# Optimization experiments

Hardware: AMD Instinct MI355X
Metric: run time of the kernel (lower is better)

## Reference

```python
import jax, jax.numpy as jnp
import numpy as np

SLOPE = 0.2  # LeakyReLU negative slope

def _mlp2(x, w1, b1, w2, b2):
    h = jax.nn.leaky_relu(x @ w1 + b1, SLOPE)
    return h @ w2 + b2

def setup_inputs() -> dict:
    key = jax.random.key(0)
    ks = jax.random.split(key, 16)
    B, N, T, A, H = 8, 512, 8, 16, 64
    D = T * A  # node_dim * timestep = 128
    s = 0.1
    return {
        "nodes": jax.random.normal(ks[0], (B, N, T, A), dtype=jnp.float32),
        "edges": jax.random.randint(ks[1], (B, N, N), 0, 2),
        "self_w1": jax.random.normal(ks[2], (D, H), dtype=jnp.float32) * s,
        "self_b1": jnp.zeros((H,), jnp.float32),
        "self_w2": jax.random.normal(ks[3], (H, H), dtype=jnp.float32) * s,
        "self_b2": jnp.zeros((H,), jnp.float32),
        "nb_w1": jax.random.normal(ks[4], (D, H), dtype=jnp.float32) * s,
        "nb_b1": jnp.zeros((H,), jnp.float32),
        "nb_w2": jax.random.normal(ks[5], (H, H), dtype=jnp.float32) * s,
        "nb_b2": jnp.zeros((H,), jnp.float32),
        "comb_w1": jax.random.normal(ks[6], (2 * H, H), dtype=jnp.float32) * s,
        "comb_b1": jnp.zeros((H,), jnp.float32),
        "comb_w2": jax.random.normal(ks[7], (H, 1), dtype=jnp.float32) * s,
        "comb_b2": jnp.zeros((1,), jnp.float32),
    }

def reference(nodes, edges, self_w1, self_b1, self_w2, self_b2,
              nb_w1, nb_b1, nb_w2, nb_b2,
              comb_w1, comb_b1, comb_w2, comb_b2):
    B, N = nodes.shape[0], nodes.shape[1]
    H = self_w2.shape[1]
    x = nodes.reshape(B, N, -1)                       # [B,N,D]
    self_e = _mlp2(x, self_w1, self_b1, self_w2, self_b2)  # [B,N,H]
    nb_e = _mlp2(x, nb_w1, nb_b1, nb_w2, nb_b2)            # [B,N,H]

    # combine_mlp(cat(self_i, nb_j)) scores; split fc1 to avoid [B,N,N,2H]
    w1_s, w1_n = comb_w1[:H], comb_w1[H:]
    pre = (jnp.einsum('bih,hk->bik', self_e, w1_s)[:, :, None, :]
           + jnp.einsum('bjh,hk->bjk', nb_e, w1_n)[:, None, :, :]
           + comb_b1)                                  # [B,N,N,H] (i=target, j=neighbor)
    scores = (jax.nn.leaky_relu(pre, SLOPE) @ comb_w2)[..., 0] + comb_b2[0]  # [B,N,N]

    # mask[b,i,j] = edges[b,j,i] != 0 and i != j
    mask = (jnp.swapaxes(edges, 1, 2) != 0) & (~jnp.eye(N, dtype=bool))
    neg = jnp.finfo(scores.dtype).min
    weights = jax.nn.softmax(jnp.where(mask, scores, neg), axis=-1)
    weights = jnp.where(mask, weights, 0.0)

    agg = jnp.einsum('bij,bjh->bih', weights, nb_e)    # weighted neighbor sum
    has_nb = mask.any(-1)                              # nodes w/o neighbors stay zero
    return jnp.where(has_nb[..., None], agg + self_e, 0.0)
```

## Files before the change

kernel.cpp:

```cpp
#include <hip/hip_runtime.h>
#include <float.h>

typedef __attribute__((ext_vector_type(8))) short short8;
typedef __attribute__((ext_vector_type(4))) float f32x4;

#define SLOPE 0.2f

__device__ __forceinline__ float leaky(float x) { return fmaxf(x, SLOPE * x); }

__device__ __forceinline__ unsigned short f2bf(float f) {
  unsigned u = __float_as_uint(f);
  return (unsigned short)((u + 0x7FFFu + ((u >> 16) & 1u)) >> 16);
}

__global__ __launch_bounds__(64) void wprep(
    const float* __restrict__ self_w1, const float* __restrict__ self_w2,
    const float* __restrict__ nb_w1,   const float* __restrict__ nb_w2,
    const float* __restrict__ comb_w1,
    unsigned short* __restrict__ wf)
{
  const int frag = blockIdx.x;
  const int lane = threadIdx.x;
  const int p = frag >> 5, fl = frag & 31;
  const float* src;
  int nt, kb;
  if (fl < 16)      { src = p ? nb_w1 : self_w1; nt = fl >> 2;        kb = fl & 3; }
  else if (fl < 24) { src = p ? nb_w2 : self_w2; nt = (fl - 16) >> 1; kb = (fl - 16) & 1; }
  else              { src = comb_w1 + p * 4096;  nt = (fl - 24) >> 1; kb = (fl - 24) & 1; }
  const int n = nt * 16 + (lane & 15);
  const int k0 = kb * 32 + (lane >> 4) * 8;
  short8 pk;
  #pragma unroll
  for (int j = 0; j < 8; ++j) pk[j] = (short)f2bf(src[(k0 + j) * 64 + n]);
  *(short8*)(wf + ((size_t)(frag * 64 + lane)) * 8) = pk;
}

__global__ __launch_bounds__(64) void mlp(
    const float* __restrict__ nodes,
    const float* __restrict__ self_b1, const float* __restrict__ self_b2,
    const float* __restrict__ nb_b1,   const float* __restrict__ nb_b2,
    const float* __restrict__ comb_b1, const float* __restrict__ comb_w2,
    const float* __restrict__ comb_b2,
    const unsigned short* __restrict__ wf,
    float* __restrict__ self_e, float* __restrict__ ss, float* __restrict__ sn,
    float* __restrict__ sP, float* __restrict__ sQ,
    unsigned short* __restrict__ nbT)
{
  __shared__ float tile[16][68];

  const int lane = threadIdx.x;
  const int arow = lane & 15, agrp = lane >> 4;
  const int node0 = blockIdx.x * 16;
  const int b = node0 >> 9, jloc = node0 & 511;

  short8 xa[4];
  {
    const float* xrow = nodes + ((size_t)(node0 + arow)) * 128 + agrp * 8;
    #pragma unroll
    for (int kb = 0; kb < 4; ++kb) {
      float v[8];
      *(float4*)&v[0] = *(const float4*)(xrow + kb * 32);
      *(float4*)&v[4] = *(const float4*)(xrow + kb * 32 + 4);
      #pragma unroll
      for (int j = 0; j < 8; ++j) xa[kb][j] = (short)f2bf(v[j]);
    }
  }

  float w2vn[4], cb1v[4];
  #pragma unroll
  for (int nt = 0; nt < 4; ++nt) {
    w2vn[nt] = comb_w2[nt * 16 + arow];
    cb1v[nt] = comb_b1[nt * 16 + arow];
  }
  const float cb2 = comb_b2[0];

  for (int p = 0; p < 2; ++p) {
    const float* b1 = p ? nb_b1 : self_b1;
    const float* b2 = p ? nb_b2 : self_b2;
    const unsigned short* wfp = wf + (size_t)p * 32 * 64 * 8;

    short8 w1f[16], w2f[8], cwf[8];
    #pragma unroll
    for (int i = 0; i < 16; ++i)
      w1f[i] = *(const short8*)(wfp + ((size_t)(i * 64 + lane)) * 8);
    #pragma unroll
    for (int i = 0; i < 8; ++i)
      w2f[i] = *(const short8*)(wfp + ((size_t)((16 + i) * 64 + lane)) * 8);
    #pragma unroll
    for (int i = 0; i < 8; ++i)
      cwf[i] = *(const short8*)(wfp + ((size_t)((24 + i) * 64 + lane)) * 8);

    f32x4 acc[4];
    #pragma unroll
    for (int nt = 0; nt < 4; ++nt) acc[nt] = (f32x4){0.f, 0.f, 0.f, 0.f};
    #pragma unroll
    for (int kb = 0; kb < 4; ++kb)
      #pragma unroll
      for (int nt = 0; nt < 4; ++nt)
        acc[nt] = __builtin_amdgcn_mfma_f32_16x16x32_bf16(xa[kb], w1f[nt * 4 + kb], acc[nt], 0, 0, 0);
    #pragma unroll
    for (int nt = 0; nt < 4; ++nt) {
      const float bv = b1[nt * 16 + arow];
      #pragma unroll
      for (int r = 0; r < 4; ++r)
        tile[agrp * 4 + r][nt * 16 + arow] = leaky(acc[nt][r] + bv);
    }

    short8 ha[2];
    #pragma unroll
    for (int kb = 0; kb < 2; ++kb) {
      float v[8];
      *(float4*)&v[0] = *(const float4*)&tile[arow][kb * 32 + agrp * 8];
      *(float4*)&v[4] = *(const float4*)&tile[arow][kb * 32 + agrp * 8 + 4];
      #pragma unroll
      for (int j = 0; j < 8; ++j) ha[kb][j] = (short)f2bf(v[j]);
    }

    #pragma unroll
    for (int nt = 0; nt < 4; ++nt) acc[nt] = (f32x4){0.f, 0.f, 0.f, 0.f};
    #pragma unroll
    for (int kb = 0; kb < 2; ++kb)
      #pragma unroll
      for (int nt = 0; nt < 4; ++nt)
        acc[nt] = __builtin_amdgcn_mfma_f32_16x16x32_bf16(ha[kb], w2f[nt * 2 + kb], acc[nt], 0, 0, 0);
    #pragma unroll
    for (int nt = 0; nt < 4; ++nt) {
      const float bv = b2[nt * 16 + arow];
      #pragma unroll
      for (int r = 0; r < 4; ++r) {
        const float ev = acc[nt][r] + bv;
        tile[agrp * 4 + r][nt * 16 + arow] = ev;
        if (p == 0)
          self_e[((size_t)(node0 + agrp * 4 + r)) * 64 + nt * 16 + arow] = ev;
      }
    }

    short8 ea[2];
    #pragma unroll
    for (int kb = 0; kb < 2; ++kb) {
      float v[8];
      *(float4*)&v[0] = *(const float4*)&tile[arow][kb * 32 + agrp * 8];
      *(float4*)&v[4] = *(const float4*)&tile[arow][kb * 32 + agrp * 8 + 4];
      #pragma unroll
      for (int j = 0; j < 8; ++j) ea[kb][j] = (short)f2bf(v[j]);
    }

    if (p == 1) {
      #pragma unroll
      for (int g = 0; g < 2; ++g) {
        short8 pk;
        #pragma unroll
        for (int jj = 0; jj < 8; ++jj)
          pk[jj] = (short)f2bf(tile[g * 8 + jj][lane]);
        *(short8*)(nbT + (size_t)b * 32768 + ((size_t)((jloc >> 3) + g)) * 512 + lane * 8) = pk;
      }
    }

    #pragma unroll
    for (int nt = 0; nt < 4; ++nt) acc[nt] = (f32x4){0.f, 0.f, 0.f, 0.f};
    #pragma unroll
    for (int kb = 0; kb < 2; ++kb)
      #pragma unroll
      for (int nt = 0; nt < 4; ++nt)
        acc[nt] = __builtin_amdgcn_mfma_f32_16x16x32_bf16(ea[kb], cwf[nt * 2 + kb], acc[nt], 0, 0, 0);

    float* so = p ? sn : ss;
    float t[4] = {0.f, 0.f, 0.f, 0.f};
    #pragma unroll
    for (int nt = 0; nt < 4; ++nt) {
      #pragma unroll
      for (int r = 0; r < 4; ++r) {
        const float sv = acc[nt][r] + (p ? 0.f : cb1v[nt]);
        so[((size_t)(node0 + agrp * 4 + r)) * 64 + nt * 16 + arow] = sv;
        t[r] += w2vn[nt] * sv;
      }
    }
    #pragma unroll
    for (int r = 0; r < 4; ++r) {
      #pragma unroll
      for (int off = 1; off < 16; off <<= 1) t[r] += __shfl_xor(t[r], off);
    }
    if (arow == 0) {
      float* po = p ? sQ : sP;
      const float add = p ? 0.f : cb2;
      #pragma unroll
      for (int r = 0; r < 4; ++r)
        po[node0 + agrp * 4 + r] = 0.6f * t[r] + add;
    }
  }
}

__global__ __launch_bounds__(512) void gat_attn(
    const int* __restrict__ edges,
    const float* __restrict__ comb_w2,
    const float* __restrict__ self_e,
    const float* __restrict__ ss, const float* __restrict__ sn,
    const float* __restrict__ sP, const float* __restrict__ sQ,
    const unsigned short* __restrict__ nbT,
    float* __restrict__ out)
{
  __shared__ __align__(16) float sn_sh[2][64][68];
  __shared__ __align__(16) unsigned short P_sh[16][520];
  __shared__ __align__(16) float red_sh[4][64][4];
  __shared__ unsigned short jm_sh[512];
  __shared__ float f_sh[16];

  const int tid = threadIdx.x, lane = tid & 63, wv = tid >> 6;
  const int b = blockIdx.x & 7, it = blockIdx.x >> 3;
  const int i0 = it * 16;
  const size_t nodeb = (size_t)b * 512;

  const int ra = wv * 2, rb = ra + 1;
  const int ia = i0 + ra, ib = ia + 1;

  const int* ebp = edges + ((size_t)(nodeb + tid)) * 512 + i0;
  const int4 ev0 = *(const int4*)(ebp + 0);
  const int4 ev1 = *(const int4*)(ebp + 4);
  const int4 ev2 = *(const int4*)(ebp + 8);
  const int4 ev3 = *(const int4*)(ebp + 12);

  float4 w2p[16], sa0[16], sa1[16];
  {
    const float4* w2v = (const float4*)comb_w2;
    const float4* s0 = (const float4*)(ss + (nodeb + ia) * 64);
    const float4* s1 = (const float4*)(ss + (nodeb + ib) * 64);
    #pragma unroll
    for (int q = 0; q < 16; ++q) {
      float4 w = w2v[q];
      w2p[q] = make_float4(0.4f * w.x, 0.4f * w.y, 0.4f * w.z, 0.4f * w.w);
      sa0[q] = s0[q];
      sa1[q] = s1[q];
    }
  }
  const float sPa = sP[nodeb + ia], sPb = sP[nodeb + ib];
  float sQv[8];
  #pragma unroll
  for (int jt = 0; jt < 8; ++jt) sQv[jt] = sQ[nodeb + jt * 64 + lane];

  {
    unsigned mj = 0;
    mj |= (ev0.x != 0 ? 1u : 0u) << 0;  mj |= (ev0.y != 0 ? 1u : 0u) << 1;
    mj |= (ev0.z != 0 ? 1u : 0u) << 2;  mj |= (ev0.w != 0 ? 1u : 0u) << 3;
    mj |= (ev1.x != 0 ? 1u : 0u) << 4;  mj |= (ev1.y != 0 ? 1u : 0u) << 5;
    mj |= (ev1.z != 0 ? 1u : 0u) << 6;  mj |= (ev1.w != 0 ? 1u : 0u) << 7;
    mj |= (ev2.x != 0 ? 1u : 0u) << 8;  mj |= (ev2.y != 0 ? 1u : 0u) << 9;
    mj |= (ev2.z != 0 ? 1u : 0u) << 10; mj |= (ev2.w != 0 ? 1u : 0u) << 11;
    mj |= (ev3.x != 0 ? 1u : 0u) << 12; mj |= (ev3.y != 0 ? 1u : 0u) << 13;
    mj |= (ev3.z != 0 ? 1u : 0u) << 14; mj |= (ev3.w != 0 ? 1u : 0u) << 15;
    const int d = tid - i0;
    if (d >= 0 && d < 16) mj &= ~(1u << d);
    jm_sh[tid] = (unsigned short)mj;
  }

  const int str = tid >> 4, stc = (tid & 15) * 4;
  const int str2 = (tid + 512) >> 4, stc2 = ((tid + 512) & 15) * 4;
  float4 st0, st1;
  {
    const float4* src = (const float4*)(sn + nodeb * 64);
    st0 = src[tid];
    st1 = src[tid + 512];
  }

  float msc0[8], msc1[8];
  int cur = 0;
  for (int jt = 0; jt < 8; ++jt) {
    *(float4*)&sn_sh[cur][str][stc] = st0;
    *(float4*)&sn_sh[cur][str2][stc2] = st1;
    if (jt < 7) {
      const float4* src = (const float4*)(sn + (nodeb + (jt + 1) * 64) * 64);
      st0 = src[tid];
      st1 = src[tid + 512];
    }
    __syncthreads();

    float acc0 = 0.f, acc1 = 0.f;
    #pragma unroll
    for (int q = 0; q < 16; ++q) {
      float4 v = *(const float4*)&sn_sh[cur][lane][q * 4];
      float4 w = w2p[q];
      float4 A = sa0[q];
      float4 Bv = sa1[q];
      acc0 += w.x * fabsf(A.x + v.x) + w.y * fabsf(A.y + v.y)
            + w.z * fabsf(A.z + v.z) + w.w * fabsf(A.w + v.w);
      acc1 += w.x * fabsf(Bv.x + v.x) + w.y * fabsf(Bv.y + v.y)
            + w.z * fabsf(Bv.z + v.z) + w.w * fabsf(Bv.w + v.w);
    }
    const unsigned mj = jm_sh[jt * 64 + lane];
    msc0[jt] = ((mj >> ra) & 1u) ? acc0 + sPa + sQv[jt] : -FLT_MAX;
    msc1[jt] = ((mj >> rb) & 1u) ? acc1 + sPb + sQv[jt] : -FLT_MAX;
    cur ^= 1;
  }

  float m0 = msc0[0], m1 = msc1[0];
  #pragma unroll
  for (int jt = 1; jt < 8; ++jt) {
    m0 = fmaxf(m0, msc0[jt]);
    m1 = fmaxf(m1, msc1[jt]);
  }
  #pragma unroll
  for (int off = 32; off; off >>= 1) {
    m0 = fmaxf(m0, __shfl_xor(m0, off));
    m1 = fmaxf(m1, __shfl_xor(m1, off));
  }

  float s0 = 0.f, s1 = 0.f;
  #pragma unroll
  for (int jt = 0; jt < 8; ++jt) {
    const float e0 = __expf(msc0[jt] - m0);
    const float e1 = __expf(msc1[jt] - m1);
    P_sh[ra][jt * 64 + lane] = f2bf(e0);
    P_sh[rb][jt * 64 + lane] = f2bf(e1);
    s0 += e0;
    s1 += e1;
  }
  #pragma unroll
  for (int off = 32; off; off >>= 1) {
    s0 += __shfl_xor(s0, off);
    s1 += __shfl_xor(s1, off);
  }
  if (lane == 0) {
    f_sh[ra] = (m0 > -1e37f) ? 1.0f / s0 : 0.0f;
    f_sh[rb] = (m1 > -1e37f) ? 1.0f / s1 : 0.0f;
  }
  __syncthreads();

  const int nt = wv & 3, kh = wv >> 2;
  const int arow = lane & 15, agrp = lane >> 4;
  const int bcol = nt * 16 + (lane & 15);
  const unsigned short* nb3 = nbT + (size_t)b * 32768 + bcol * 8;

  f32x4 C = {0.f, 0.f, 0.f, 0.f};
  #pragma unroll
  for (int ks = 0; ks < 8; ++ks) {
    const int jb = kh * 256 + ks * 32 + agrp * 8;
    short8 afr = *(const short8*)&P_sh[arow][jb];
    short8 bfr = *(const short8*)(nb3 + (size_t)jb * 64);
    C = __builtin_amdgcn_mfma_f32_16x16x32_bf16(afr, bfr, C, 0, 0, 0);
  }
  if (kh == 1) *(f32x4*)&red_sh[wv - 4][lane][0] = C;
  __syncthreads();
  if (kh == 0) {
    f32x4 P = *(const f32x4*)&red_sh[wv][lane][0];
    #pragma unroll
    for (int r = 0; r < 4; ++r) {
      const int rg = agrp * 4 + r;
      const float f = f_sh[rg];
      const size_t adr = (nodeb + i0 + rg) * 64 + bcol;
      const float val = (C[r] + P[r]) * f + self_e[adr];
      out[adr] = (f > 0.f) ? val : 0.f;
    }
  }
}

extern "C" void kernel_launch(void* const* d_in, const int* in_sizes, int n_in,
                              void* d_out, int out_size, void* d_ws, size_t ws_size,
                              hipStream_t stream) {
  const float* nodes   = (const float*)d_in[0];
  const int*   edges   = (const int*)  d_in[1];
  const float* self_w1 = (const float*)d_in[2];
  const float* self_b1 = (const float*)d_in[3];
  const float* self_w2 = (const float*)d_in[4];
  const float* self_b2 = (const float*)d_in[5];
  const float* nb_w1   = (const float*)d_in[6];
  const float* nb_b1   = (const float*)d_in[7];
  const float* nb_w2   = (const float*)d_in[8];
  const float* nb_b2   = (const float*)d_in[9];
  const float* comb_w1 = (const float*)d_in[10];
  const float* comb_b1 = (const float*)d_in[11];
  const float* comb_w2 = (const float*)d_in[12];
  const float* comb_b2 = (const float*)d_in[13];

  float* ws     = (float*)d_ws;
  float* self_e = ws;
  float* ss     = ws + 262144;
  float* sn     = ws + 524288;
  float* sP     = ws + 786432;
  float* sQ     = ws + 790528;
  unsigned short* nbT = (unsigned short*)(ws + 794624);
  unsigned short* wf  = (unsigned short*)(ws + 925696);

  wprep<<<64, 64, 0, stream>>>(self_w1, self_w2, nb_w1, nb_w2, comb_w1, wf);

  mlp<<<256, 64, 0, stream>>>(
      nodes, self_b1, self_b2, nb_b1, nb_b2, comb_b1, comb_w2, comb_b2,
      wf, self_e, ss, sn, sP, sQ, nbT);

  gat_attn<<<256, 512, 0, stream>>>(
      edges, comb_w2, self_e, ss, sn, sP, sQ, nbT, (float*)d_out);
}
```

Baseline: 34.62 us.

## Store neighbor scores as packed bf16 pairs, register-resident per thread in attention

```diff
diff --git a/kernel.cpp b/kernel.cpp
--- a/kernel.cpp
+++ b/kernel.cpp
@@ -42,7 +42,8 @@
     const float* __restrict__ comb_b1, const float* __restrict__ comb_w2,
     const float* __restrict__ comb_b2,
     const unsigned short* __restrict__ wf,
-    float* __restrict__ self_e, float* __restrict__ ss, float* __restrict__ sn,
+    float* __restrict__ self_e, float* __restrict__ ss,
+    unsigned* __restrict__ snP,
     float* __restrict__ sP, float* __restrict__ sQ,
     unsigned short* __restrict__ nbT)
 {
@@ -164,14 +165,16 @@
       for (int nt = 0; nt < 4; ++nt)
         acc[nt] = __builtin_amdgcn_mfma_f32_16x16x32_bf16(ea[kb], cwf[nt * 2 + kb], acc[nt], 0, 0, 0);
 
-    float* so = p ? sn : ss;
     float t[4] = {0.f, 0.f, 0.f, 0.f};
     #pragma unroll
     for (int nt = 0; nt < 4; ++nt) {
       #pragma unroll
       for (int r = 0; r < 4; ++r) {
         const float sv = acc[nt][r] + (p ? 0.f : cb1v[nt]);
-        so[((size_t)(node0 + agrp * 4 + r)) * 64 + nt * 16 + arow] = sv;
+        if (p == 0)
+          ss[((size_t)(node0 + agrp * 4 + r)) * 64 + nt * 16 + arow] = sv;
+        else
+          tile[agrp * 4 + r][nt * 16 + arow] = sv;
         t[r] += w2vn[nt] * sv;
       }
     }
@@ -186,6 +189,17 @@
       #pragma unroll
       for (int r = 0; r < 4; ++r)
         po[node0 + agrp * 4 + r] = 0.6f * t[r] + add;
+    }
+
+    if (p == 1) {
+      const int kp = lane & 31, half = lane >> 5;
+      #pragma unroll
+      for (int g = 0; g < 8; ++g) {
+        const int n = half * 8 + g;
+        const unsigned pkv = (unsigned)f2bf(tile[n][2 * kp])
+                           | ((unsigned)f2bf(tile[n][2 * kp + 1]) << 16);
+        snP[((size_t)(b * 32 + kp)) * 512 + jloc + n] = pkv;
+      }
     }
   }
 }
@@ -194,15 +208,17 @@
     const int* __restrict__ edges,
     const float* __restrict__ comb_w2,
     const float* __restrict__ self_e,
-    const float* __restrict__ ss, const float* __restrict__ sn,
+    const float* __restrict__ ss, const unsigned* __restrict__ snP,
     const float* __restrict__ sP, const float* __restrict__ sQ,
     const unsigned short* __restrict__ nbT,
     float* __restrict__ out)
 {
-  __shared__ __align__(16) float sn_sh[2][64][68];
+  __shared__ __align__(16) float sc_sh[16][512];
   __shared__ __align__(16) unsigned short P_sh[16][520];
   __shared__ __align__(16) float red_sh[4][64][4];
-  __shared__ unsigned short jm_sh[512];
+  __shared__ float rmax_sh[8][16];
+  __shared__ float rsum_sh[8][16];
+  __shared__ float mx_sh[16];
   __shared__ float f_sh[16];
 
   const int tid = threadIdx.x, lane = tid & 63, wv = tid >> 6;
@@ -210,34 +226,20 @@
   const int i0 = it * 16;
   const size_t nodeb = (size_t)b * 512;
 
-  const int ra = wv * 2, rb = ra + 1;
-  const int ia = i0 + ra, ib = ia + 1;
-
-  const int* ebp = edges + ((size_t)(nodeb + tid)) * 512 + i0;
-  const int4 ev0 = *(const int4*)(ebp + 0);
-  const int4 ev1 = *(const int4*)(ebp + 4);
-  const int4 ev2 = *(const int4*)(ebp + 8);
-  const int4 ev3 = *(const int4*)(ebp + 12);
-
-  float4 w2p[16], sa0[16], sa1[16];
+  unsigned snv[32];
+  #pragma unroll
+  for (int kp = 0; kp < 32; ++kp)
+    snv[kp] = snP[((size_t)(b * 32 + kp)) * 512 + tid];
+
+  const float sQj = sQ[nodeb + tid];
+
+  unsigned emask;
   {
-    const float4* w2v = (const float4*)comb_w2;
-    const float4* s0 = (const float4*)(ss + (nodeb + ia) * 64);
-    const float4* s1 = (const float4*)(ss + (nodeb + ib) * 64);
-    #pragma unroll
-    for (int q = 0; q < 16; ++q) {
-      float4 w = w2v[q];
-      w2p[q] = make_float4(0.4f * w.x, 0.4f * w.y, 0.4f * w.z, 0.4f * w.w);
-      sa0[q] = s0[q];
-      sa1[q] = s1[q];
-    }
-  }
-  const float sPa = sP[nodeb + ia], sPb = sP[nodeb + ib];
-  float sQv[8];
-  #pragma unroll
-  for (int jt = 0; jt < 8; ++jt) sQv[jt] = sQ[nodeb + jt * 64 + lane];
-
-  {
+    const int* ebp = edges + ((size_t)(nodeb + tid)) * 512 + i0;
+    const int4 ev0 = *(const int4*)(ebp + 0);
+    const int4 ev1 = *(const int4*)(ebp + 4);
+    const int4 ev2 = *(const int4*)(ebp + 8);
+    const int4 ev3 = *(const int4*)(ebp + 12);
     unsigned mj = 0;
     mj |= (ev0.x != 0 ? 1u : 0u) << 0;  mj |= (ev0.y != 0 ? 1u : 0u) << 1;
     mj |= (ev0.z != 0 ? 1u : 0u) << 2;  mj |= (ev0.w != 0 ? 1u : 0u) << 3;
@@ -249,78 +251,59 @@
     mj |= (ev3.z != 0 ? 1u : 0u) << 14; mj |= (ev3.w != 0 ? 1u : 0u) << 15;
     const int d = tid - i0;
     if (d >= 0 && d < 16) mj &= ~(1u << d);
-    jm_sh[tid] = (unsigned short)mj;
-  }
-
-  const int str = tid >> 4, stc = (tid & 15) * 4;
-  const int str2 = (tid + 512) >> 4, stc2 = ((tid + 512) & 15) * 4;
-  float4 st0, st1;
-  {
-    const float4* src = (const float4*)(sn + nodeb * 64);
-    st0 = src[tid];
-    st1 = src[tid + 512];
-  }
-
-  float msc0[8], msc1[8];
-  int cur = 0;
-  for (int jt = 0; jt < 8; ++jt) {
-    *(float4*)&sn_sh[cur][str][stc] = st0;
-    *(float4*)&sn_sh[cur][str2][stc2] = st1;
-    if (jt < 7) {
-      const float4* src = (const float4*)(sn + (nodeb + (jt + 1) * 64) * 64);
-      st0 = src[tid];
-      st1 = src[tid + 512];
-    }
-    __syncthreads();
-
-    float acc0 = 0.f, acc1 = 0.f;
-    #pragma unroll
-    for (int q = 0; q < 16; ++q) {
-      float4 v = *(const float4*)&sn_sh[cur][lane][q * 4];
-      float4 w = w2p[q];
-      float4 A = sa0[q];
-      float4 Bv = sa1[q];
-      acc0 += w.x * fabsf(A.x + v.x) + w.y * fabsf(A.y + v.y)
-            + w.z * fabsf(A.z + v.z) + w.w * fabsf(A.w + v.w);
-      acc1 += w.x * fabsf(Bv.x + v.x) + w.y * fabsf(Bv.y + v.y)
-            + w.z * fabsf(Bv.z + v.z) + w.w * fabsf(Bv.w + v.w);
-    }
-    const unsigned mj = jm_sh[jt * 64 + lane];
-    msc0[jt] = ((mj >> ra) & 1u) ? acc0 + sPa + sQv[jt] : -FLT_MAX;
-    msc1[jt] = ((mj >> rb) & 1u) ? acc1 + sPb + sQv[jt] : -FLT_MAX;
-    cur ^= 1;
-  }
-
-  float m0 = msc0[0], m1 = msc1[0];
-  #pragma unroll
-  for (int jt = 1; jt < 8; ++jt) {
-    m0 = fmaxf(m0, msc0[jt]);
-    m1 = fmaxf(m1, msc1[jt]);
-  }
-  #pragma unroll
-  for (int off = 32; off; off >>= 1) {
-    m0 = fmaxf(m0, __shfl_xor(m0, off));
-    m1 = fmaxf(m1, __shfl_xor(m1, off));
-  }
-
-  float s0 = 0.f, s1 = 0.f;
-  #pragma unroll
-  for (int jt = 0; jt < 8; ++jt) {
-    const float e0 = __expf(msc0[jt] - m0);
-    const float e1 = __expf(msc1[jt] - m1);
-    P_sh[ra][jt * 64 + lane] = f2bf(e0);
-    P_sh[rb][jt * 64 + lane] = f2bf(e1);
-    s0 += e0;
-    s1 += e1;
-  }
-  #pragma unroll
-  for (int off = 32; off; off >>= 1) {
-    s0 += __shfl_xor(s0, off);
-    s1 += __shfl_xor(s1, off);
-  }
-  if (lane == 0) {
-    f_sh[ra] = (m0 > -1e37f) ? 1.0f / s0 : 0.0f;
-    f_sh[rb] = (m1 > -1e37f) ? 1.0f / s1 : 0.0f;
+    emask = mj;
+  }
+
+  float w2v[64];
+  #pragma unroll
+  for (int q = 0; q < 16; ++q)
+    *(float4*)&w2v[q * 4] = ((const float4*)comb_w2)[q];
+
+  for (int i = 0; i < 16; ++i) {
+    const float* ssr = ss + (nodeb + i0 + i) * 64;
+    float a0 = 0.f, a1 = 0.f;
+    #pragma unroll
+    for (int kp = 0; kp < 32; ++kp) {
+      const unsigned pk = snv[kp];
+      const float e0 = __uint_as_float(pk << 16);
+      const float e1 = __uint_as_float(pk & 0xffff0000u);
+      const float t0 = ssr[2 * kp] + e0;
+      const float t1 = ssr[2 * kp + 1] + e1;
+      a0 = fmaf(w2v[2 * kp], fabsf(t0), a0);
+      a1 = fmaf(w2v[2 * kp + 1], fabsf(t1), a1);
+    }
+    float sc = (a0 + a1) * 0.4f + sP[nodeb + i0 + i] + sQj;
+    sc = ((emask >> i) & 1u) ? sc : -FLT_MAX;
+    sc_sh[i][tid] = sc;
+    float m = sc;
+    #pragma unroll
+    for (int off = 32; off; off >>= 1) m = fmaxf(m, __shfl_xor(m, off));
+    if (lane == 0) rmax_sh[wv][i] = m;
+  }
+  __syncthreads();
+  if (tid < 16) {
+    float m = rmax_sh[0][tid];
+    #pragma unroll
+    for (int w = 1; w < 8; ++w) m = fmaxf(m, rmax_sh[w][tid]);
+    mx_sh[tid] = m;
+  }
+  __syncthreads();
+
+  #pragma unroll
+  for (int i = 0; i < 16; ++i) {
+    const float e = __expf(sc_sh[i][tid] - mx_sh[i]);
+    P_sh[i][tid] = f2bf(e);
+    float s = e;
+    #pragma unroll
+    for (int off = 32; off; off >>= 1) s += __shfl_xor(s, off);
+    if (lane == 0) rsum_sh[wv][i] = s;
+  }
+  __syncthreads();
+  if (tid < 16) {
+    float s = rsum_sh[0][tid];
+    #pragma unroll
+    for (int w = 1; w < 8; ++w) s += rsum_sh[w][tid];
+    f_sh[tid] = (mx_sh[tid] > -1e37f) ? 1.0f / s : 0.0f;
   }
   __syncthreads();
 
@@ -373,7 +356,7 @@
   float* ws     = (float*)d_ws;
   float* self_e = ws;
   float* ss     = ws + 262144;
-  float* sn     = ws + 524288;
+  unsigned* snP = (unsigned*)(ws + 524288);
   float* sP     = ws + 786432;
   float* sQ     = ws + 790528;
   unsigned short* nbT = (unsigned short*)(ws + 794624);
@@ -383,8 +366,8 @@
 
   mlp<<<256, 64, 0, stream>>>(
       nodes, self_b1, self_b2, nb_b1, nb_b2, comb_b1, comb_w2, comb_b2,
-      wf, self_e, ss, sn, sP, sQ, nbT);
+      wf, self_e, ss, snP, sP, sQ, nbT);
 
   gat_attn<<<256, 512, 0, stream>>>(
-      edges, comb_w2, self_e, ss, sn, sP, sQ, nbT, (float*)d_out);
-}
+      edges, comb_w2, self_e, ss, snP, sP, sQ, nbT, (float*)d_out);
+}
```

Result: slower. 51.55 us (+48.9%).
